# Optimization experiments

Measured on AMD Instinct MI355X. Metric: run time of the kernel, lower is better.

## Reference

```python
import jax, jax.numpy as jnp
import numpy as np

QUERY_DIM, FEAT_DIM, HID_DIM, OUT_DIM = 512, 2048, 512, 512
B, L, S, T = 8, 128, 100, 100


def setup_inputs() -> dict:
    key = jax.random.key(0)
    ks = jax.random.split(key, 9)
    d = {
        "query": jax.random.normal(ks[0], (B, L, QUERY_DIM), jnp.float32),
        "src": jax.random.normal(ks[1], (B, S, FEAT_DIM), jnp.float32),
        "trg": jax.random.normal(ks[2], (B, T, FEAT_DIM), jnp.float32),
        # params (LinearAct == Linear + identity act); src/trg projections share weights
        "Wq": jax.random.normal(ks[3], (QUERY_DIM, HID_DIM), jnp.float32) / np.sqrt(QUERY_DIM),
        "bq": jnp.zeros((HID_DIM,), jnp.float32),
        "Ws": jax.random.normal(ks[4], (FEAT_DIM, HID_DIM), jnp.float32) / np.sqrt(FEAT_DIM),
        "bs": jnp.zeros((HID_DIM,), jnp.float32),
        "Wo": jax.random.normal(ks[5], (HID_DIM + QUERY_DIM, OUT_DIM), jnp.float32) / np.sqrt(HID_DIM + QUERY_DIM),
        "bo": jnp.zeros((OUT_DIM,), jnp.float32),
    }
    return d


def reference(query, src, trg, Wq, bq, Ws, bs, Wo, bo):
    b, l, _ = query.shape
    s = src.shape[1]
    t = trg.shape[1]
    q = query @ Wq + bq          # b,l,k
    s_key = src @ Ws + bs        # b,s,k
    t_key = trg @ Ws + bs        # b,t,k
    hid = q.shape[-1]
    # score[b,l,s,t] = q . (s_key - t_key)/sqrt(2) / sqrt(hid) -- decomposed, no b,s,t,k tensor
    qs = jnp.einsum('blk,bsk->bls', q, s_key)
    qt = jnp.einsum('blk,btk->blt', q, t_key)
    score = (qs[:, :, :, None] - qt[:, :, None, :]) / jnp.sqrt(jnp.asarray(2.0 * hid, q.dtype))
    w = jax.nn.softmax(score.reshape(b, l, s * t), axis=-1).reshape(b, l, s, t)
    # ctx = sum_{s,t} w * (s_key - t_key)/sqrt(2), decomposed via marginals
    ws = w.sum(axis=3)           # b,l,s
    wt = w.sum(axis=2)           # b,l,t
    ctx = (jnp.einsum('bls,bsk->blk', ws, s_key) - jnp.einsum('blt,btk->blk', wt, t_key)) / jnp.sqrt(jnp.asarray(2.0, q.dtype))
    x = jnp.concatenate([query, ctx], axis=-1) @ Wo + bo
    return x
```

## Files before the change

### kernel.cpp

```cpp
#include <hip/hip_runtime.h>
#include <math.h>


typedef __attribute__((ext_vector_type(8))) short s16x8;
typedef __attribute__((ext_vector_type(4))) float f32x4;

__device__ __forceinline__ unsigned short f2bf(float f) {
    unsigned int u = __float_as_uint(f);
    return (unsigned short)((u + 0x7fffu + ((u >> 16) & 1u)) >> 16);
}

__global__ __launch_bounds__(256) void k_prep(
    const float* __restrict__ query, const float* __restrict__ src,
    const float* __restrict__ trg, const float* __restrict__ Wq,
    const float* __restrict__ Ws, const float* __restrict__ Wo,
    const float* __restrict__ bs, const float* __restrict__ bo,
    unsigned short* __restrict__ qbf, unsigned short* __restrict__ aout,
    unsigned short* __restrict__ abf, unsigned short* __restrict__ WqT,
    unsigned short* __restrict__ WsT, unsigned short* __restrict__ WoT,
    float* __restrict__ keys, float* __restrict__ out) {
    __shared__ float tile[32][33];
    const int bid = blockIdx.x, t = threadIdx.x;

    if (bid < 3712) {
        const int idx = bid * 256 + t;
        if (idx < 131072) {
            float4 v = *(const float4*)(query + (size_t)idx * 4);
            ushort4 o = make_ushort4(f2bf(v.x), f2bf(v.y), f2bf(v.z), f2bf(v.w));
            *(ushort4*)(qbf + (size_t)idx * 4) = o;
            const int flat = idx * 4, m = flat >> 9, c = flat & 511;
            *(ushort4*)(aout + (size_t)m * 1024 + c) = o;
        } else if (idx < 540672) {
            const int i = idx - 131072;
            float4 v = *(const float4*)(src + (size_t)i * 4);
            *(ushort4*)(abf + (size_t)i * 4) =
                make_ushort4(f2bf(v.x), f2bf(v.y), f2bf(v.z), f2bf(v.w));
        } else {
            const int i = idx - 540672;
            float4 v = *(const float4*)(trg + (size_t)i * 4);
            *(ushort4*)(abf + 1638400 + (size_t)i * 4) =
                make_ushort4(f2bf(v.x), f2bf(v.y), f2bf(v.z), f2bf(v.w));
        }
    } else if (bid < 5504) {
        const int id = bid - 3712;
        const float* W; unsigned short* O; int K, tk, tn;
        if (id < 256)       { W = Wq; O = WqT; K = 512;  tk = id >> 4;          tn = id & 15; }
        else if (id < 1280) { W = Ws; O = WsT; K = 2048; tk = (id - 256) >> 4;  tn = (id - 256) & 15; }
        else                { W = Wo; O = WoT; K = 1024; tk = (id - 1280) >> 4; tn = (id - 1280) & 15; }
        const int row = t >> 3, c4 = (t & 7) * 4;
        float4 v = *(const float4*)(W + (size_t)(tk * 32 + row) * 512 + tn * 32 + c4);
        tile[row][c4 + 0] = v.x; tile[row][c4 + 1] = v.y;
        tile[row][c4 + 2] = v.z; tile[row][c4 + 3] = v.w;
        __syncthreads();
        ushort4 o = make_ushort4(f2bf(tile[c4 + 0][row]), f2bf(tile[c4 + 1][row]),
                                 f2bf(tile[c4 + 2][row]), f2bf(tile[c4 + 3][row]));
        *(ushort4*)(O + (size_t)(tn * 32 + row) * K + tk * 32 + c4) = o;
    } else if (bid < 6304) {
        const int f = ((bid - 5504) * 256 + t) * 4;
        *(float4*)(keys + f) = *(const float4*)(bs + (f & 511));
    } else {
        const int f = ((bid - 6304) * 256 + t) * 4;
        *(float4*)(out + f) = *(const float4*)(bo + (f & 511));
    }
}


__device__ __forceinline__ void gemm64_atomic(
    const unsigned short* __restrict__ A, const unsigned short* __restrict__ BT,
    float* __restrict__ C, int m0, int n0, int K, int N, int kbase, int kiters,
    unsigned short* As, unsigned short* Bs) {
    const int t = threadIdx.x;
    const int lane = t & 63, wid = t >> 6;
    const int wm = (wid & 1) * 32, wn = (wid >> 1) * 32;
    const int lr = lane & 15, lq = lane >> 4;
    const int r = t >> 3, c8 = (t & 7) * 8;

    s16x8 ra0, ra1, rb0, rb1;
#define LD64(kt)                                                           \
    ra0 = *(const s16x8*)(A  + (size_t)(m0 + r)      * K + (kt) + c8);     \
    ra1 = *(const s16x8*)(A  + (size_t)(m0 + r + 32) * K + (kt) + c8);     \
    rb0 = *(const s16x8*)(BT + (size_t)(n0 + r)      * K + (kt) + c8);     \
    rb1 = *(const s16x8*)(BT + (size_t)(n0 + r + 32) * K + (kt) + c8);

    f32x4 acc[2][2] = {};
    LD64(kbase);
    for (int it = 0; it < kiters; it++) {
        __syncthreads();
        *(s16x8*)&As[r * 72 + c8]        = ra0;
        *(s16x8*)&As[(r + 32) * 72 + c8] = ra1;
        *(s16x8*)&Bs[r * 72 + c8]        = rb0;
        *(s16x8*)&Bs[(r + 32) * 72 + c8] = rb1;
        __syncthreads();
        if (it + 1 < kiters) { LD64(kbase + (it + 1) * 64); }
#pragma unroll
        for (int s = 0; s < 2; s++) {
            s16x8 a0 = *(const s16x8*)&As[(wm + lr) * 72      + s * 32 + lq * 8];
            s16x8 a1 = *(const s16x8*)&As[(wm + 16 + lr) * 72 + s * 32 + lq * 8];
            s16x8 b0 = *(const s16x8*)&Bs[(wn + lr) * 72      + s * 32 + lq * 8];
            s16x8 b1 = *(const s16x8*)&Bs[(wn + 16 + lr) * 72 + s * 32 + lq * 8];
            acc[0][0] = __builtin_amdgcn_mfma_f32_16x16x32_bf16(a0, b0, acc[0][0], 0, 0, 0);
            acc[0][1] = __builtin_amdgcn_mfma_f32_16x16x32_bf16(a0, b1, acc[0][1], 0, 0, 0);
            acc[1][0] = __builtin_amdgcn_mfma_f32_16x16x32_bf16(a1, b0, acc[1][0], 0, 0, 0);
            acc[1][1] = __builtin_amdgcn_mfma_f32_16x16x32_bf16(a1, b1, acc[1][1], 0, 0, 0);
        }
    }
#undef LD64
#pragma unroll
    for (int i = 0; i < 2; i++)
#pragma unroll
        for (int j = 0; j < 2; j++) {
            const int col = n0 + wn + j * 16 + lr;
            const int row = m0 + wm + i * 16 + lq * 4;
#pragma unroll
            for (int rr = 0; rr < 4; rr++)
                unsafeAtomicAdd(&C[(size_t)(row + rr) * N + col], acc[i][j][rr]);
        }
}

template <bool ATOMIC>
__device__ __forceinline__ void gemm32(
    const unsigned short* __restrict__ A, const unsigned short* __restrict__ BT,
    const float* __restrict__ bias, float* __restrict__ C,
    int m0, int n0, int K, int N, int kbase, int kiters,
    unsigned short* As, unsigned short* Bs) {
    const int t = threadIdx.x;
    const int lane = t & 63, wid = t >> 6;
    const int wm = (wid & 1) * 16, wn = (wid >> 1) * 32;
    const int lr = lane & 15, lq = lane >> 4;
    const int r = t >> 3, c8 = (t & 7) * 8;

    s16x8 ra, rb0, rb1;
#define LD32(kt)                                                           \
    ra  = *(const s16x8*)(A  + (size_t)(m0 + r)      * K + (kt) + c8);     \
    rb0 = *(const s16x8*)(BT + (size_t)(n0 + r)      * K + (kt) + c8);     \
    rb1 = *(const s16x8*)(BT + (size_t)(n0 + r + 32) * K + (kt) + c8);

    f32x4 acc[2] = {};
    LD32(kbase);
    for (int it = 0; it < kiters; it++) {
        __syncthreads();
        *(s16x8*)&As[r * 72 + c8]        = ra;
        *(s16x8*)&Bs[r * 72 + c8]        = rb0;
        *(s16x8*)&Bs[(r + 32) * 72 + c8] = rb1;
        __syncthreads();
        if (it + 1 < kiters) { LD32(kbase + (it + 1) * 64); }
#pragma unroll
        for (int s = 0; s < 2; s++) {
            s16x8 a0 = *(const s16x8*)&As[(wm + lr) * 72      + s * 32 + lq * 8];
            s16x8 b0 = *(const s16x8*)&Bs[(wn + lr) * 72      + s * 32 + lq * 8];
            s16x8 b1 = *(const s16x8*)&Bs[(wn + 16 + lr) * 72 + s * 32 + lq * 8];
            acc[0] = __builtin_amdgcn_mfma_f32_16x16x32_bf16(a0, b0, acc[0], 0, 0, 0);
            acc[1] = __builtin_amdgcn_mfma_f32_16x16x32_bf16(a0, b1, acc[1], 0, 0, 0);
        }
    }
#undef LD32
#pragma unroll
    for (int j = 0; j < 2; j++) {
        const int col = n0 + wn + j * 16 + lr;
        const int row = m0 + wm + lq * 4;
        if (ATOMIC) {
#pragma unroll
            for (int rr = 0; rr < 4; rr++)
                unsafeAtomicAdd(&C[(size_t)(row + rr) * N + col], acc[j][rr]);
        } else {
            const float bv = bias[col];
#pragma unroll
            for (int rr = 0; rr < 4; rr++)
                C[(size_t)(row + rr) * N + col] = acc[j][rr] + bv;
        }
    }
}

__global__ __launch_bounds__(256) void k_stageB(
    const unsigned short* __restrict__ qbf, const unsigned short* __restrict__ abf,
    const unsigned short* __restrict__ WqT, const unsigned short* __restrict__ WsT,
    const float* __restrict__ bq, float* __restrict__ q, float* __restrict__ keys) {
    __shared__ __align__(16) unsigned short As[64 * 72];
    __shared__ __align__(16) unsigned short Bs[64 * 72];
    const int bid = blockIdx.x;
    if (bid < 800) {
        const int c = bid / 200, rem = bid % 200;
        const int mt = rem >> 3, nt = rem & 7;
        gemm64_atomic(abf, WsT, keys, mt * 64, nt * 64, 2048, 512, c * 512, 8, As, Bs);
    } else {
        const int r = bid - 800;
        const int mt = r >> 3, nt = r & 7;
        gemm32<false>(qbf, WqT, bq, q, mt * 32, nt * 64, 512, 512, 0, 8, As, Bs);
    }
}

__global__ __launch_bounds__(256) void k_out(
    const unsigned short* __restrict__ aout, const unsigned short* __restrict__ WoT,
    float* __restrict__ out) {
    __shared__ __align__(16) unsigned short As[64 * 72];
    __shared__ __align__(16) unsigned short Bs[64 * 72];
    const int bid = blockIdx.x;
    const int c = bid >> 8, rem = bid & 255;
    const int mt = rem >> 3, nt = rem & 7;
    gemm32<true>(aout, WoT, nullptr, out, mt * 32, nt * 64, 1024, 512,
                 c * 512, 8, As, Bs);
}

__global__ __launch_bounds__(256) void k_scores(
    const float* __restrict__ q, const float* __restrict__ keys,
    float* __restrict__ wsT, float* __restrict__ wtT) {
    __shared__ __align__(16) float qsh[512];
    __shared__ float sc[200];

    const int t = threadIdx.x;
    const int row = blockIdx.x;
    const int b = row >> 7, l = row & 127;

    if (t < 128)
        *(float4*)&qsh[t * 4] = *(const float4*)(q + (size_t)row * 512 + t * 4);
    __syncthreads();

    const int wave = t >> 6, lane = t & 63;
    const float4* qp = (const float4*)qsh;
    const float4 qv1 = qp[lane], qv2 = qp[lane + 64];

    for (int idx = wave; idx < 200; idx += 4) {
        const int kr = (idx < 100) ? (b * 100 + idx)
                                   : (800 + b * 100 + (idx - 100));
        const float4* kp = (const float4*)(keys + (size_t)kr * 512);
        const float4 kv1 = kp[lane], kv2 = kp[lane + 64];
        float d = kv1.x * qv1.x + kv1.y * qv1.y + kv1.z * qv1.z + kv1.w * qv1.w
                + kv2.x * qv2.x + kv2.y * qv2.y + kv2.z * qv2.z + kv2.w * qv2.w;
#pragma unroll
        for (int off = 32; off > 0; off >>= 1) d += __shfl_down(d, off);
        if (lane == 0)
            sc[idx] = ((idx < 100) ? d : -d) * (1.0f / 32.0f);
    }
    __syncthreads();

    if (wave < 2) {
        const float* sp = sc + wave * 100;
        const bool hi = (lane + 64) < 100;
        const float v0 = sp[lane];
        const float v1 = hi ? sp[lane + 64] : -INFINITY;
        float mx = fmaxf(v0, v1);
#pragma unroll
        for (int off = 32; off > 0; off >>= 1) mx = fmaxf(mx, __shfl_xor(mx, off));
        const float e0 = __expf(v0 - mx);
        const float e1 = hi ? __expf(v1 - mx) : 0.f;
        float s = e0 + e1;
#pragma unroll
        for (int off = 32; off > 0; off >>= 1) s += __shfl_xor(s, off);
        const float inv = 1.f / s;
        float* op = (wave == 0) ? wsT : wtT;
        op[(b * 100 + lane) * 128 + l] = e0 * inv;
        if (hi) op[(b * 100 + lane + 64) * 128 + l] = e1 * inv;
    }
}

__global__ __launch_bounds__(256) void k_ctx(
    const float* __restrict__ wsT, const float* __restrict__ wtT,
    const float* __restrict__ keys, unsigned short* __restrict__ aout) {
    __shared__ float As[40][32];
    __shared__ float Bs[40][32];

    const int t = threadIdx.x;
    const int b = blockIdx.y;
    const int n0 = blockIdx.x * 32;
    const int l0 = blockIdx.z * 32;
    const int tx = t & 7, ty = t >> 3;

    float rA[5], rB[5];
    auto loadc = [&](int kbase) {
#pragma unroll
        for (int e = 0; e < 5; e++) {
            const int idx = t + e * 256;
            const int k = idx >> 5, j = idx & 31;
            const int kk = kbase + k;
            rA[e] = (kk < 100) ? wsT[(b * 100 + kk) * 128 + l0 + j]
                               : wtT[(b * 100 + (kk - 100)) * 128 + l0 + j];
            rB[e] = (kk < 100)
                ?  keys[(size_t)(b * 100 + kk) * 512 + n0 + j]
                : -keys[(size_t)(800 + b * 100 + (kk - 100)) * 512 + n0 + j];
        }
    };

    float acc[4] = {};
    loadc(0);
    for (int c5 = 0; c5 < 5; c5++) {
        __syncthreads();
#pragma unroll
        for (int e = 0; e < 5; e++) {
            const int idx = t + e * 256;
            As[idx >> 5][idx & 31] = rA[e];
            Bs[idx >> 5][idx & 31] = rB[e];
        }
        __syncthreads();
        if (c5 < 4) loadc((c5 + 1) * 40);
#pragma unroll 8
        for (int k = 0; k < 40; k++) {
            const float ar = As[k][ty];
            float br[4];
            *(float4*)br = *(const float4*)&Bs[k][tx * 4];
#pragma unroll
            for (int j = 0; j < 4; j++) acc[j] = fmaf(ar, br[j], acc[j]);
        }
    }

    const float s2 = 0.70710678118654752f;
    const int m = b * 128 + l0 + ty;
    ushort4 o = make_ushort4(f2bf(acc[0] * s2), f2bf(acc[1] * s2),
                             f2bf(acc[2] * s2), f2bf(acc[3] * s2));
    *(ushort4*)(aout + (size_t)m * 1024 + 512 + n0 + tx * 4) = o;
}


extern "C" void kernel_launch(void* const* d_in, const int* in_sizes, int n_in,
                              void* d_out, int out_size, void* d_ws, size_t ws_size,
                              hipStream_t stream) {
    const float* query = (const float*)d_in[0];
    const float* src   = (const float*)d_in[1];
    const float* trg   = (const float*)d_in[2];
    const float* Wq    = (const float*)d_in[3];
    const float* bq    = (const float*)d_in[4];
    const float* Ws    = (const float*)d_in[5];
    const float* bs    = (const float*)d_in[6];
    const float* Wo    = (const float*)d_in[7];
    const float* bo    = (const float*)d_in[8];
    float* out = (float*)d_out;

    float* q    = (float*)d_ws;
    float* keys = q    + 524288;
    float* wsT  = keys + 819200;
    float* wtT  = wsT  + 102400;
    unsigned short* qbf = (unsigned short*)(wtT + 102400);
    unsigned short* abf = qbf + 524288;
    unsigned short* aout= abf + 3276800;
    unsigned short* wqt = aout + 1048576;
    unsigned short* wst = wqt  + 262144;
    unsigned short* wot = wst  + 1048576;

    k_prep<<<6816, 256, 0, stream>>>(query, src, trg, Wq, Ws, Wo, bs, bo,
                                     qbf, aout, abf, wqt, wst, wot, keys, out);
    k_stageB<<<1056, 256, 0, stream>>>(qbf, abf, wqt, wst, bq, q, keys);
    k_scores<<<1024, 256, 0, stream>>>(q, keys, wsT, wtT);
    k_ctx<<<dim3(16, 8, 4), 256, 0, stream>>>(wsT, wtT, keys, aout);
    k_out<<<512, 256, 0, stream>>>(aout, wot, out);
}
```

Baseline: 150.4 us.

## Compute attention scores with bf16 MFMA GEMM and fuse softmax into ctx kernel

Replaces the per-row scalar dot-product score kernel with a split-K bf16 MFMA GEMM that writes scaled scores atomically into a zero-initialised buffer. The q projection is now stored as bf16, and the keys are converted to bf16 on the fly. The softmax over the s and t marginals moves into the ctx kernel, which holds the normalised weights in shared memory, so the separate wsT/wtT round trip is gone. In exchange, score precision drops to bf16 inputs, the softmax is recomputed redundantly by each of the 16 column blocks, and atomics add contention.

```diff
diff --git a/kernel.cpp b/kernel.cpp
--- a/kernel.cpp
+++ b/kernel.cpp
@@ -18,7 +18,7 @@
     unsigned short* __restrict__ qbf, unsigned short* __restrict__ aout,
     unsigned short* __restrict__ abf, unsigned short* __restrict__ WqT,
     unsigned short* __restrict__ WsT, unsigned short* __restrict__ WoT,
-    float* __restrict__ keys, float* __restrict__ out) {
+    float* __restrict__ keys, float* __restrict__ out, float* __restrict__ sc) {
     __shared__ float tile[32][33];
     const int bid = blockIdx.x, t = threadIdx.x;
 
@@ -58,9 +58,12 @@
     } else if (bid < 6304) {
         const int f = ((bid - 5504) * 256 + t) * 4;
         *(float4*)(keys + f) = *(const float4*)(bs + (f & 511));
-    } else {
+    } else if (bid < 6816) {
         const int f = ((bid - 6304) * 256 + t) * 4;
         *(float4*)(out + f) = *(const float4*)(bo + (f & 511));
+    } else {
+        const int f = ((bid - 6816) * 256 + t) * 4;
+        *(float4*)(sc + f) = make_float4(0.f, 0.f, 0.f, 0.f);
     }
 }
 
@@ -117,10 +120,10 @@
         }
 }
 
-template <bool ATOMIC>
+template <int MODE>
 __device__ __forceinline__ void gemm32(
     const unsigned short* __restrict__ A, const unsigned short* __restrict__ BT,
-    const float* __restrict__ bias, float* __restrict__ C,
+    const float* __restrict__ bias, void* __restrict__ Cv,
     int m0, int n0, int K, int N, int kbase, int kiters,
     unsigned short* As, unsigned short* Bs) {
     const int t = threadIdx.x;
@@ -158,15 +161,23 @@
     for (int j = 0; j < 2; j++) {
         const int col = n0 + wn + j * 16 + lr;
         const int row = m0 + wm + lq * 4;
-        if (ATOMIC) {
+        if (MODE == 1) {
+            float* C = (float*)Cv;
 #pragma unroll
             for (int rr = 0; rr < 4; rr++)
                 unsafeAtomicAdd(&C[(size_t)(row + rr) * N + col], acc[j][rr]);
-        } else {
+        } else if (MODE == 0) {
+            float* C = (float*)Cv;
             const float bv = bias[col];
 #pragma unroll
             for (int rr = 0; rr < 4; rr++)
                 C[(size_t)(row + rr) * N + col] = acc[j][rr] + bv;
+        } else {
+            unsigned short* C = (unsigned short*)Cv;
+            const float bv = bias[col];
+#pragma unroll
+            for (int rr = 0; rr < 4; rr++)
+                C[(size_t)(row + rr) * N + col] = f2bf(acc[j][rr] + bv);
         }
     }
 }
@@ -174,7 +185,8 @@
 __global__ __launch_bounds__(256) void k_stageB(
     const unsigned short* __restrict__ qbf, const unsigned short* __restrict__ abf,
     const unsigned short* __restrict__ WqT, const unsigned short* __restrict__ WsT,
-    const float* __restrict__ bq, float* __restrict__ q, float* __restrict__ keys) {
+    const float* __restrict__ bq, unsigned short* __restrict__ qh,
+    float* __restrict__ keys) {
     __shared__ __align__(16) unsigned short As[64 * 72];
     __shared__ __align__(16) unsigned short Bs[64 * 72];
     const int bid = blockIdx.x;
@@ -185,8 +197,172 @@
     } else {
         const int r = bid - 800;
         const int mt = r >> 3, nt = r & 7;
-        gemm32<false>(qbf, WqT, bq, q, mt * 32, nt * 64, 512, 512, 0, 8, As, Bs);
-    }
+        gemm32<2>(qbf, WqT, bq, qh, mt * 32, nt * 64, 512, 512, 0, 8, As, Bs);
+    }
+}
+
+__global__ __launch_bounds__(256) void k_scgemm(
+    const unsigned short* __restrict__ qh, const float* __restrict__ keys,
+    float* __restrict__ sc) {
+    __shared__ __align__(16) unsigned short As[32 * 72];
+    __shared__ __align__(16) unsigned short Bs[64 * 72];
+    const int bid = blockIdx.x;
+    const int c = bid >> 7, rem = bid & 127;
+    const int mt = rem >> 2, nt = rem & 3;
+    const int m0 = mt * 32, b = mt >> 2, n0 = nt * 64;
+    const int kbase = c * 256;
+    const int t = threadIdx.x;
+    const int lane = t & 63, wid = t >> 6;
+    const int wm = (wid & 1) * 16, wn = (wid >> 1) * 32;
+    const int lr = lane & 15, lq = lane >> 4;
+    const int r = t >> 3, c8 = (t & 7) * 8;
+
+    const int nA = n0 + r, nB = n0 + r + 32;
+    int kr0 = (nA < 128) ? (b * 100 + nA) : (800 + b * 100 + (nA - 128));
+    int kr1 = (nB < 128) ? (b * 100 + nB) : (800 + b * 100 + (nB - 128));
+    kr0 = kr0 > 1599 ? 1599 : kr0;
+    kr1 = kr1 > 1599 ? 1599 : kr1;
+
+    s16x8 ra, rb0, rb1;
+    auto cvt8 = [](const float* p) {
+        float4 u = *(const float4*)p, w = *(const float4*)(p + 4);
+        s16x8 o;
+        o[0] = (short)f2bf(u.x); o[1] = (short)f2bf(u.y);
+        o[2] = (short)f2bf(u.z); o[3] = (short)f2bf(u.w);
+        o[4] = (short)f2bf(w.x); o[5] = (short)f2bf(w.y);
+        o[6] = (short)f2bf(w.z); o[7] = (short)f2bf(w.w);
+        return o;
+    };
+#define LDSC(kt)                                                   \
+    ra  = *(const s16x8*)(qh + (size_t)(m0 + r) * 512 + (kt) + c8); \
+    rb0 = cvt8(keys + (size_t)kr0 * 512 + (kt) + c8);               \
+    rb1 = cvt8(keys + (size_t)kr1 * 512 + (kt) + c8);
+
+    f32x4 acc[2] = {};
+    LDSC(kbase);
+    for (int it = 0; it < 4; it++) {
+        __syncthreads();
+        *(s16x8*)&As[r * 72 + c8]        = ra;
+        *(s16x8*)&Bs[r * 72 + c8]        = rb0;
+        *(s16x8*)&Bs[(r + 32) * 72 + c8] = rb1;
+        __syncthreads();
+        if (it < 3) { LDSC(kbase + (it + 1) * 64); }
+#pragma unroll
+        for (int s = 0; s < 2; s++) {
+            s16x8 a0 = *(const s16x8*)&As[(wm + lr) * 72      + s * 32 + lq * 8];
+            s16x8 b0 = *(const s16x8*)&Bs[(wn + lr) * 72      + s * 32 + lq * 8];
+            s16x8 b1 = *(const s16x8*)&Bs[(wn + 16 + lr) * 72 + s * 32 + lq * 8];
+            acc[0] = __builtin_amdgcn_mfma_f32_16x16x32_bf16(a0, b0, acc[0], 0, 0, 0);
+            acc[1] = __builtin_amdgcn_mfma_f32_16x16x32_bf16(a0, b1, acc[1], 0, 0, 0);
+        }
+    }
+#undef LDSC
+#pragma unroll
+    for (int j = 0; j < 2; j++) {
+        const int col = n0 + wn + j * 16 + lr;
+        const int row = m0 + wm + lq * 4;
+        const float scale = (col >= 128) ? -(1.0f / 32.0f) : (1.0f / 32.0f);
+#pragma unroll
+        for (int rr = 0; rr < 4; rr++)
+            unsafeAtomicAdd(&sc[(size_t)(row + rr) * 256 + col],
+                            acc[j][rr] * scale);
+    }
+}
+
+__global__ __launch_bounds__(256) void k_ctx(
+    const float* __restrict__ sc, const float* __restrict__ keys,
+    unsigned short* __restrict__ aout) {
+    __shared__ float wbuf[200 * 33];
+    __shared__ float Bs[40 * 32];
+
+    const int t = threadIdx.x;
+    const int b = blockIdx.y;
+    const int n0 = blockIdx.x * 32;
+    const int l0 = blockIdx.z * 32;
+    const int wave = t >> 6, lane = t & 63;
+
+    for (int i = 0; i < 8; i++) {
+        const int li = wave * 8 + i;
+        const float4 v = *(const float4*)(
+            sc + (size_t)(b * 128 + l0 + li) * 256 + lane * 4);
+        const float vv[4] = {v.x, v.y, v.z, v.w};
+        const int c0 = lane * 4;
+        float mS = -1e30f, mT = -1e30f;
+#pragma unroll
+        for (int j = 0; j < 4; j++) {
+            const int col = c0 + j;
+            if (col < 100) mS = fmaxf(mS, vv[j]);
+            if (col >= 128 && col < 228) mT = fmaxf(mT, vv[j]);
+        }
+#pragma unroll
+        for (int off = 32; off > 0; off >>= 1) {
+            mS = fmaxf(mS, __shfl_xor(mS, off));
+            mT = fmaxf(mT, __shfl_xor(mT, off));
+        }
+        float eS[4], eT[4], sS = 0.f, sT = 0.f;
+#pragma unroll
+        for (int j = 0; j < 4; j++) {
+            const int col = c0 + j;
+            eS[j] = (col < 100) ? __expf(vv[j] - mS) : 0.f;
+            eT[j] = (col >= 128 && col < 228) ? __expf(vv[j] - mT) : 0.f;
+            sS += eS[j]; sT += eT[j];
+        }
+#pragma unroll
+        for (int off = 32; off > 0; off >>= 1) {
+            sS += __shfl_xor(sS, off);
+            sT += __shfl_xor(sT, off);
+        }
+        const float iS = 1.f / sS, iT = 1.f / sT;
+#pragma unroll
+        for (int j = 0; j < 4; j++) {
+            const int col = c0 + j;
+            if (col < 100) wbuf[col * 33 + li] = eS[j] * iS;
+            if (col >= 128 && col < 228)
+                wbuf[(100 + col - 128) * 33 + li] = eT[j] * iT;
+        }
+    }
+    __syncthreads();
+
+    const int tx = t & 7, ty = t >> 3;
+    float rB[5];
+    auto loadB = [&](int kbase) {
+#pragma unroll
+        for (int e = 0; e < 5; e++) {
+            const int idx = t + e * 256;
+            const int k = idx >> 5, j = idx & 31;
+            const int kk = kbase + k;
+            rB[e] = (kk < 100)
+                ?  keys[(size_t)(b * 100 + kk) * 512 + n0 + j]
+                : -keys[(size_t)(800 + b * 100 + (kk - 100)) * 512 + n0 + j];
+        }
+    };
+
+    float acc[4] = {};
+    loadB(0);
+    for (int c5 = 0; c5 < 5; c5++) {
+        __syncthreads();
+#pragma unroll
+        for (int e = 0; e < 5; e++) {
+            const int idx = t + e * 256;
+            Bs[idx] = rB[e];
+        }
+        __syncthreads();
+        if (c5 < 4) loadB((c5 + 1) * 40);
+#pragma unroll 8
+        for (int k = 0; k < 40; k++) {
+            const float ar = wbuf[(c5 * 40 + k) * 33 + ty];
+            float br[4];
+            *(float4*)br = *(const float4*)&Bs[k * 32 + tx * 4];
+#pragma unroll
+            for (int j = 0; j < 4; j++) acc[j] = fmaf(ar, br[j], acc[j]);
+        }
+    }
+
+    const float s2 = 0.70710678118654752f;
+    const int m = b * 128 + l0 + ty;
+    ushort4 o = make_ushort4(f2bf(acc[0] * s2), f2bf(acc[1] * s2),
+                             f2bf(acc[2] * s2), f2bf(acc[3] * s2));
+    *(ushort4*)(aout + (size_t)m * 1024 + 512 + n0 + tx * 4) = o;
 }
 
 __global__ __launch_bounds__(256) void k_out(
@@ -197,116 +373,8 @@
     const int bid = blockIdx.x;
     const int c = bid >> 8, rem = bid & 255;
     const int mt = rem >> 3, nt = rem & 7;
-    gemm32<true>(aout, WoT, nullptr, out, mt * 32, nt * 64, 1024, 512,
-                 c * 512, 8, As, Bs);
-}
-
-__global__ __launch_bounds__(256) void k_scores(
-    const float* __restrict__ q, const float* __restrict__ keys,
-    float* __restrict__ wsT, float* __restrict__ wtT) {
-    __shared__ __align__(16) float qsh[512];
-    __shared__ float sc[200];
-
-    const int t = threadIdx.x;
-    const int row = blockIdx.x;
-    const int b = row >> 7, l = row & 127;
-
-    if (t < 128)
-        *(float4*)&qsh[t * 4] = *(const float4*)(q + (size_t)row * 512 + t * 4);
-    __syncthreads();
-
-    const int wave = t >> 6, lane = t & 63;
-    const float4* qp = (const float4*)qsh;
-    const float4 qv1 = qp[lane], qv2 = qp[lane + 64];
-
-    for (int idx = wave; idx < 200; idx += 4) {
-        const int kr = (idx < 100) ? (b * 100 + idx)
-                                   : (800 + b * 100 + (idx - 100));
-        const float4* kp = (const float4*)(keys + (size_t)kr * 512);
-        const float4 kv1 = kp[lane], kv2 = kp[lane + 64];
-        float d = kv1.x * qv1.x + kv1.y * qv1.y + kv1.z * qv1.z + kv1.w * qv1.w
-                + kv2.x * qv2.x + kv2.y * qv2.y + kv2.z * qv2.z + kv2.w * qv2.w;
-#pragma unroll
-        for (int off = 32; off > 0; off >>= 1) d += __shfl_down(d, off);
-        if (lane == 0)
-            sc[idx] = ((idx < 100) ? d : -d) * (1.0f / 32.0f);
-    }
-    __syncthreads();
-
-    if (wave < 2) {
-        const float* sp = sc + wave * 100;
-        const bool hi = (lane + 64) < 100;
-        const float v0 = sp[lane];
-        const float v1 = hi ? sp[lane + 64] : -INFINITY;
-        float mx = fmaxf(v0, v1);
-#pragma unroll
-        for (int off = 32; off > 0; off >>= 1) mx = fmaxf(mx, __shfl_xor(mx, off));
-        const float e0 = __expf(v0 - mx);
-        const float e1 = hi ? __expf(v1 - mx) : 0.f;
-        float s = e0 + e1;
-#pragma unroll
-        for (int off = 32; off > 0; off >>= 1) s += __shfl_xor(s, off);
-        const float inv = 1.f / s;
-        float* op = (wave == 0) ? wsT : wtT;
-        op[(b * 100 + lane) * 128 + l] = e0 * inv;
-        if (hi) op[(b * 100 + lane + 64) * 128 + l] = e1 * inv;
-    }
-}
-
-__global__ __launch_bounds__(256) void k_ctx(
-    const float* __restrict__ wsT, const float* __restrict__ wtT,
-    const float* __restrict__ keys, unsigned short* __restrict__ aout) {
-    __shared__ float As[40][32];
-    __shared__ float Bs[40][32];
-
-    const int t = threadIdx.x;
-    const int b = blockIdx.y;
-    const int n0 = blockIdx.x * 32;
-    const int l0 = blockIdx.z * 32;
-    const int tx = t & 7, ty = t >> 3;
-
-    float rA[5], rB[5];
-    auto loadc = [&](int kbase) {
-#pragma unroll
-        for (int e = 0; e < 5; e++) {
-            const int idx = t + e * 256;
-            const int k = idx >> 5, j = idx & 31;
-            const int kk = kbase + k;
-            rA[e] = (kk < 100) ? wsT[(b * 100 + kk) * 128 + l0 + j]
-                               : wtT[(b * 100 + (kk - 100)) * 128 + l0 + j];
-            rB[e] = (kk < 100)
-                ?  keys[(size_t)(b * 100 + kk) * 512 + n0 + j]
-                : -keys[(size_t)(800 + b * 100 + (kk - 100)) * 512 + n0 + j];
-        }
-    };
-
-    float acc[4] = {};
-    loadc(0);
-    for (int c5 = 0; c5 < 5; c5++) {
-        __syncthreads();
-#pragma unroll
-        for (int e = 0; e < 5; e++) {
-            const int idx = t + e * 256;
-            As[idx >> 5][idx & 31] = rA[e];
-            Bs[idx >> 5][idx & 31] = rB[e];
-        }
-        __syncthreads();
-        if (c5 < 4) loadc((c5 + 1) * 40);
-#pragma unroll 8
-        for (int k = 0; k < 40; k++) {
-            const float ar = As[k][ty];
-            float br[4];
-            *(float4*)br = *(const float4*)&Bs[k][tx * 4];
-#pragma unroll
-            for (int j = 0; j < 4; j++) acc[j] = fmaf(ar, br[j], acc[j]);
-        }
-    }
-
-    const float s2 = 0.70710678118654752f;
-    const int m = b * 128 + l0 + ty;
-    ushort4 o = make_ushort4(f2bf(acc[0] * s2), f2bf(acc[1] * s2),
-                             f2bf(acc[2] * s2), f2bf(acc[3] * s2));
-    *(ushort4*)(aout + (size_t)m * 1024 + 512 + n0 + tx * 4) = o;
+    gemm32<1>(aout, WoT, nullptr, out, mt * 32, nt * 64, 1024, 512,
+              c * 512, 8, As, Bs);
 }
 
 
@@ -324,21 +392,21 @@
     const float* bo    = (const float*)d_in[8];
     float* out = (float*)d_out;
 
-    float* q    = (float*)d_ws;
-    float* keys = q    + 524288;
-    float* wsT  = keys + 819200;
-    float* wtT  = wsT  + 102400;
-    unsigned short* qbf = (unsigned short*)(wtT + 102400);
-    unsigned short* abf = qbf + 524288;
+    float* keys = (float*)d_ws;
+    float* sc   = keys + 819200;
+    unsigned short* qbf = (unsigned short*)(sc + 262144);
+    unsigned short* qh  = qbf + 524288;
+    unsigned short* abf = qh  + 524288;
     unsigned short* aout= abf + 3276800;
     unsigned short* wqt = aout + 1048576;
     unsigned short* wst = wqt  + 262144;
     unsigned short* wot = wst  + 1048576;
 
-    k_prep<<<6816, 256, 0, stream>>>(query, src, trg, Wq, Ws, Wo, bs, bo,
-                                     qbf, aout, abf, wqt, wst, wot, keys, out);
-    k_stageB<<<1056, 256, 0, stream>>>(qbf, abf, wqt, wst, bq, q, keys);
-    k_scores<<<1024, 256, 0, stream>>>(q, keys, wsT, wtT);
-    k_ctx<<<dim3(16, 8, 4), 256, 0, stream>>>(wsT, wtT, keys, aout);
+    k_prep<<<7072, 256, 0, stream>>>(query, src, trg, Wq, Ws, Wo, bs, bo,
+                                     qbf, aout, abf, wqt, wst, wot,
+                                     keys, out, sc);
+    k_stageB<<<1056, 256, 0, stream>>>(qbf, abf, wqt, wst, bq, qh, keys);
+    k_scgemm<<<256, 256, 0, stream>>>(qh, keys, sc);
+    k_ctx<<<dim3(16, 8, 4), 256, 0, stream>>>(sc, keys, aout);
     k_out<<<512, 256, 0, stream>>>(aout, wot, out);
 }
```

Result: faster. 132.7 us (-11.8%).
